# Optimization experiments

Hardware: AMD Instinct MI355X
Metric: run time of the kernel (lower is better)

## Reference

```python
import jax, jax.numpy as jnp
import numpy as np

N = 100000      # nodes
E = 400000      # edges (before self loops)
D_ATOM = 98
D_BOND = 13
EMB = 128
HEADS = 4
L = 4           # num_layer


def prelu(x, a):
    return jnp.where(x >= 0, x, a * x)


def setup_inputs() -> dict:
    key = jax.random.key(0)
    ks = jax.random.split(key, 12)
    s = 0.05
    inp = {
        "x": jax.random.normal(ks[0], (N, D_ATOM), dtype=jnp.float32),
        "edge_index": jax.random.randint(ks[1], (2, E), 0, N, dtype=jnp.int64),
        "edge_attr": jax.random.uniform(ks[2], (E, D_BOND), dtype=jnp.float32),
        # GNN-level params
        "x_emb_W": jax.random.normal(ks[3], (D_ATOM, EMB), dtype=jnp.float32) * s,
        "prelu_gnn": jnp.float32(0.25),
        # per-layer GATConv params, stacked on leading layer axis
        "wl_W": jax.random.normal(ks[4], (L, EMB, HEADS * EMB), dtype=jnp.float32) * s,
        "wl_b": jnp.zeros((L, HEADS * EMB), dtype=jnp.float32),
        "att": jax.random.normal(ks[5], (L, HEADS, 2 * EMB), dtype=jnp.float32) * s,
        "gat_bias": jnp.zeros((L, EMB), dtype=jnp.float32),
        "ee_W": jax.random.normal(ks[6], (L, D_BOND, HEADS * EMB), dtype=jnp.float32) * s,
        "ee_b": jnp.zeros((L, HEADS * EMB), dtype=jnp.float32),
        "prelu_gat": jnp.full((L,), 0.25, dtype=jnp.float32),
        # LayerNorm params per layer
        "ln_g": jnp.ones((L, EMB), dtype=jnp.float32),
        "ln_b": jnp.zeros((L, EMB), dtype=jnp.float32),
    }
    return inp


def reference(x, edge_index, edge_attr, x_emb_W, prelu_gnn, wl_W, wl_b, att,
              gat_bias, ee_W, ee_b, prelu_gat, ln_g, ln_b):
    # add self loops: (i, i) for every node; self-loop edge_attr = zeros
    loop = jnp.arange(N, dtype=edge_index.dtype)
    src = jnp.concatenate([edge_index[0], loop])  # [E+N] source (j)
    dst = jnp.concatenate([edge_index[1], loop])  # [E+N] target (i)
    ea = jnp.concatenate(
        [edge_attr, jnp.zeros((N, D_BOND), dtype=edge_attr.dtype)], axis=0)

    # input embedding + shared PReLU
    h = prelu(x @ x_emb_W, prelu_gnn)  # [N, EMB]

    for l in range(L):
        a = prelu_gat[l]
        ee = prelu(ea @ ee_W[l] + ee_b[l], a)       # [E+N, H*EMB]
        xw = prelu(h @ wl_W[l] + wl_b[l], a)        # [N, H*EMB]
        x_i = xw[dst].reshape(-1, HEADS, EMB)       # target feats
        x_j = (xw[src] + ee).reshape(-1, HEADS, EMB)  # source feats + edge emb
        # attention logits: cat([x_i,x_j]) . att
        alpha = (x_i * att[l, :, :EMB]).sum(-1) + (x_j * att[l, :, EMB:]).sum(-1)
        alpha = prelu(alpha, a)                     # [E+N, HEADS]
        # segment softmax grouped by src (edge_index[0]), as in the module
        m = jax.ops.segment_max(alpha, src, num_segments=N)
        alpha = jnp.exp(alpha - m[src])
        ssum = jax.ops.segment_sum(alpha, src, num_segments=N)
        alpha = alpha / (ssum[src] + 1e-16)
        # weighted messages, scatter-add to target nodes
        msg = (x_j * alpha[:, :, None]).reshape(-1, HEADS * EMB)
        aggr = jax.ops.segment_sum(msg, dst, num_segments=N)
        aggr = aggr.reshape(N, HEADS, EMB).mean(axis=1) + gat_bias[l]
        # LayerNorm
        mu = aggr.mean(-1, keepdims=True)
        var = ((aggr - mu) ** 2).mean(-1, keepdims=True)
        hn = (aggr - mu) / jnp.sqrt(var + 1e-5) * ln_g[l] + ln_b[l]
        # dropout is identity (drop_ratio=0); PReLU on all but last layer
        h = hn if l == L - 1 else prelu(hn, prelu_gnn)

    return h  # JK='last'
```

## Files before the change

kernel.cpp:

```cpp
#include <hip/hip_runtime.h>
#include <stdint.h>

#define NN 100000
#define NE 400000
#define NT 500000
#define DA 98
#define DB 13
#define EMB 128
#define HE 512
#define NWAVE 8192

typedef unsigned short ushort_t;
typedef __bf16 bf16x8 __attribute__((ext_vector_type(8)));
typedef float floatx4 __attribute__((ext_vector_type(4)));
typedef __fp16 fp16v2 __attribute__((ext_vector_type(2)));

__device__ __forceinline__ float prelu_f(float x, float a) { return x >= 0.f ? x : a * x; }

__device__ __forceinline__ ushort_t f2bf(float f) {
    unsigned u = __float_as_uint(f);
    unsigned r = (u + 0x7fffu + ((u >> 16) & 1u)) >> 16;
    return (ushort_t)r;
}
__device__ __forceinline__ float bflo(unsigned u) { return __uint_as_float(u << 16); }
__device__ __forceinline__ float bfhi(unsigned u) { return __uint_as_float(u & 0xffff0000u); }

__device__ __forceinline__ float dot2(unsigned a, unsigned b, float c) {
    return __builtin_amdgcn_fdot2(__builtin_bit_cast(fp16v2, a), __builtin_bit_cast(fp16v2, b), c, false);
}

__device__ __forceinline__ unsigned pk2(float lo, float hi) {
    fp16v2 p = __builtin_amdgcn_cvt_pkrtz(lo, hi);
    return __builtin_bit_cast(unsigned, p);
}

__global__ void k_count(const int* __restrict__ ei, int* __restrict__ sc, int* __restrict__ dc) {
    int e = blockIdx.x * 256 + threadIdx.x;
    if (e >= NT) return;
    int s, d;
    if (e < NE) { s = ei[e]; d = ei[NE + e]; } else { s = d = e - NE; }
    atomicAdd(sc + s, 1);
    atomicAdd(dc + d, 1);
}

__global__ void k_scan1(const int* __restrict__ cnt, int* __restrict__ part, int* __restrict__ bsum) {
    __shared__ int tmp[512];
    int t = threadIdx.x, i = blockIdx.x * 512 + t;
    int v = (i < NN) ? cnt[i] : 0;
    tmp[t] = v;
    __syncthreads();
    for (int off = 1; off < 512; off <<= 1) {
        int x = (t >= off) ? tmp[t - off] : 0;
        __syncthreads();
        tmp[t] += x;
        __syncthreads();
    }
    if (i < NN) part[i] = tmp[t] - v;
    if (t == 511) bsum[blockIdx.x] = tmp[t];
}

__global__ void k_scan2(int* __restrict__ bsum, int nb) {
    __shared__ int tmp[256];
    int t = threadIdx.x;
    int v = (t < nb) ? bsum[t] : 0;
    tmp[t] = v;
    __syncthreads();
    for (int off = 1; off < 256; off <<= 1) {
        int x = (t >= off) ? tmp[t - off] : 0;
        __syncthreads();
        tmp[t] += x;
        __syncthreads();
    }
    if (t < nb) bsum[t] = tmp[t] - v;
}

__global__ void k_scan3(const int* __restrict__ part, const int* __restrict__ bsum,
                        int* __restrict__ off, int* __restrict__ cur) {
    int i = blockIdx.x * 256 + threadIdx.x;
    if (i < NN) {
        int v = part[i] + bsum[i >> 9];
        off[i] = v;
        cur[i] = v;
    }
    if (i == 0) off[NN] = NT;
}

__global__ void k_fill(const int* __restrict__ ei, int* __restrict__ scur, int* __restrict__ dcur,
                       int* __restrict__ seid, int* __restrict__ deid) {
    int e = blockIdx.x * 256 + threadIdx.x;
    if (e >= NT) return;
    int s, d;
    if (e < NE) { s = ei[e]; d = ei[NE + e]; } else { s = d = e - NE; }
    seid[atomicAdd(scur + s, 1)] = e;
    deid[atomicAdd(dcur + d, 1)] = e;
}

__global__ void k_invperm(const int* __restrict__ seid, int* __restrict__ s2p) {
    int i = blockIdx.x * 256 + threadIdx.x;
    if (i < NT) s2p[seid[i]] = i;
}

__global__ void k_wrange(const int* __restrict__ doff, int* __restrict__ nstart) {
    int w = blockIdx.x * 256 + threadIdx.x;
    if (w > NWAVE) return;
    long long target = (long long)w * NT / NWAVE;
    int lo = 0, hi = NN;
    while (lo < hi) {
        int mid = (lo + hi) >> 1;
        if ((long long)doff[mid] < target) lo = mid + 1; else hi = mid;
    }
    nstart[w] = lo;
}

__global__ void k_dprep(const int* __restrict__ deid, const int* __restrict__ ei,
                        const float* __restrict__ ea, const int* __restrict__ s2p,
                        int* __restrict__ src_d, int* __restrict__ d2s,
                        unsigned* __restrict__ ea_d) {
    int i = blockIdx.x * 256 + threadIdx.x;
    if (i >= NT) return;
    int eid = deid[i];
    unsigned p[8] = {0, 0, 0, 0, 0, 0, 0, 0};
    int s;
    if (eid < NE) {
        s = ei[eid];
        float v[DB];
        #pragma unroll
        for (int k = 0; k < DB; ++k) v[k] = ea[(size_t)eid * DB + k];
        #pragma unroll
        for (int kp = 0; kp < 6; ++kp) p[kp] = pk2(v[2 * kp], v[2 * kp + 1]);
        p[6] = pk2(v[12], 0.f);
    } else {
        s = eid - NE;
    }
    uint4* o = (uint4*)&ea_d[(size_t)i * 8];
    o[0] = make_uint4(p[0], p[1], p[2], p[3]);
    o[1] = make_uint4(p[4], p[5], p[6], p[7]);
    src_d[i] = s;
    d2s[i] = s2p[eid];
}

__global__ __launch_bounds__(128) void k_embed(const float* __restrict__ x, const float* __restrict__ W,
                                               const float* __restrict__ pg, ushort_t* __restrict__ hb) {
    __shared__ float Ws[DA * EMB];
    __shared__ float xr[DA];
    int t = threadIdx.x;
    for (int i = t; i < DA * EMB; i += 128) Ws[i] = W[i];
    float p = pg[0];
    __syncthreads();
    for (int n = blockIdx.x; n < NN; n += gridDim.x) {
        if (t < DA) xr[t] = x[(size_t)n * DA + t];
        __syncthreads();
        float acc = 0.f;
        #pragma unroll
        for (int k = 0; k < DA; ++k) acc += xr[k] * Ws[k * EMB + t];
        hb[(size_t)n * EMB + t] = f2bf(prelu_f(acc, p));
        __syncthreads();
    }
}

__global__ void k_prep(const float* __restrict__ wlW, ushort_t* __restrict__ Wtg) {
    int idx = blockIdx.x * 256 + threadIdx.x;
    if (idx >= 4 * 512 * 128) return;
    int k = idx & 127;
    int n = (idx >> 7) & 511;
    int l = idx >> 16;
    Wtg[idx] = f2bf(wlW[(size_t)l * 65536 + k * 512 + n]);
}

__global__ void k_prep_eep(const float* __restrict__ eeW, unsigned* __restrict__ eeWp) {
    int idx = blockIdx.x * 256 + threadIdx.x;
    if (idx >= 4 * 7 * 512) return;
    int l = idx / 3584;
    int rem = idx - l * 3584;
    int kp = rem >> 9;
    int ch = rem & 511;
    float lo = eeW[((size_t)l * DB + 2 * kp) * HE + ch];
    float hi = (2 * kp + 1 < DB) ? eeW[((size_t)l * DB + 2 * kp + 1) * HE + ch] : 0.f;
    eeWp[idx] = pk2(lo, hi);
}

__global__ __launch_bounds__(256) void k_gemm(const ushort_t* __restrict__ hb, const ushort_t* __restrict__ Wtg,
                                              const float* __restrict__ bl, const float* __restrict__ pa,
                                              ushort_t* __restrict__ xw) {
    __shared__ ushort_t At[64 * 136];
    __shared__ ushort_t Bt[128 * 136];
    int t = threadIdx.x;
    int m0 = blockIdx.x * 64;
    int n0 = blockIdx.y * 128;
    for (int idx = t; idx < 64 * 16; idx += 256) {
        int r = idx >> 4, co = (idx & 15) * 8;
        int gr = m0 + r; if (gr >= NN) gr = 0;
        *(uint4*)&At[r * 136 + co] = *(const uint4*)&hb[(size_t)gr * EMB + co];
    }
    for (int idx = t; idx < 128 * 16; idx += 256) {
        int n = idx >> 4, ko = (idx & 15) * 8;
        *(uint4*)&Bt[n * 136 + ko] = *(const uint4*)&Wtg[(size_t)(n0 + n) * 128 + ko];
    }
    float a = pa[0];
    __syncthreads();

    int wv = t >> 6, lane = t & 63;
    int ml = lane & 15, kq = lane >> 4;
    int n0w = wv * 32;
    floatx4 acc[4][2];
    #pragma unroll
    for (int mt = 0; mt < 4; ++mt)
        #pragma unroll
        for (int nt = 0; nt < 2; ++nt)
            acc[mt][nt] = (floatx4){0.f, 0.f, 0.f, 0.f};

    #pragma unroll
    for (int k0 = 0; k0 < 128; k0 += 32) {
        bf16x8 af[4], bfv[2];
        #pragma unroll
        for (int mt = 0; mt < 4; ++mt) {
            uint4 u = *(const uint4*)&At[(mt * 16 + ml) * 136 + k0 + kq * 8];
            af[mt] = __builtin_bit_cast(bf16x8, u);
        }
        #pragma unroll
        for (int nt = 0; nt < 2; ++nt) {
            uint4 u = *(const uint4*)&Bt[(n0w + nt * 16 + ml) * 136 + k0 + kq * 8];
            bfv[nt] = __builtin_bit_cast(bf16x8, u);
        }
        #pragma unroll
        for (int mt = 0; mt < 4; ++mt)
            #pragma unroll
            for (int nt = 0; nt < 2; ++nt)
                acc[mt][nt] = __builtin_amdgcn_mfma_f32_16x16x32_bf16(af[mt], bfv[nt], acc[mt][nt], 0, 0, 0);
    }
    #pragma unroll
    for (int nt = 0; nt < 2; ++nt) {
        int col = n0 + n0w + nt * 16 + ml;
        float bv = bl[col];
        #pragma unroll
        for (int mt = 0; mt < 4; ++mt) {
            int row = m0 + mt * 16 + kq * 4;
            #pragma unroll
            for (int q = 0; q < 4; ++q) {
                int r = row + q;
                if (r < NN) xw[(size_t)r * HE + col] = f2bf(prelu_f(acc[mt][nt][q] + bv, a));
            }
        }
    }
}

__global__ __launch_bounds__(256) void k_dots(const ushort_t* __restrict__ xw,
                                              const float* __restrict__ attl,
                                              float* __restrict__ ddst, float* __restrict__ dsrc) {
    int t = threadIdx.x;
    int lane = t & 63;
    int wid = blockIdx.x * 4 + (t >> 6);
    int nw = gridDim.x * 4;
    int hd = lane >> 4;
    int cm = (lane & 15) * 8;
    float a1[8], a2[8];
    #pragma unroll
    for (int q = 0; q < 8; ++q) {
        a1[q] = attl[hd * 256 + cm + q];
        a2[q] = attl[hd * 256 + 128 + cm + q];
    }
    for (int n = wid; n < NN; n += nw) {
        uint4 u = *(const uint4*)&xw[(size_t)n * HE + lane * 8];
        float v[8] = {bflo(u.x), bfhi(u.x), bflo(u.y), bfhi(u.y),
                      bflo(u.z), bfhi(u.z), bflo(u.w), bfhi(u.w)};
        float p1 = 0.f, p2 = 0.f;
        #pragma unroll
        for (int q = 0; q < 8; ++q) { p1 += v[q] * a1[q]; p2 += v[q] * a2[q]; }
        #pragma unroll
        for (int m = 1; m < 16; m <<= 1) {
            p1 += __shfl_xor(p1, m, 64);
            p2 += __shfl_xor(p2, m, 64);
        }
        if ((lane & 15) == 0) {
            ddst[n * 4 + hd] = p1;
            dsrc[n * 4 + hd] = p2;
        }
    }
}

__global__ __launch_bounds__(256) void k_edge(const int* __restrict__ ei, const float* __restrict__ ea,
                                              const unsigned* __restrict__ eeWp, const float* __restrict__ ebl,
                                              const float* __restrict__ attl, const float* __restrict__ pa,
                                              const float* __restrict__ ddst, const float* __restrict__ dsrc,
                                              const int* __restrict__ s2p,
                                              float* __restrict__ alpha_s) {
    int t = threadIdx.x;
    float a = pa[0];
    int lane = t & 63;
    int wid = blockIdx.x * 4 + (t >> 6);
    int nw = gridDim.x * 4;
    int hd = lane >> 4;
    int cm = (lane & 15) * 8;
    int c0 = lane * 8;
    uint4 wpa[7], wpb[7];
    #pragma unroll
    for (int kp = 0; kp < 7; ++kp) {
        wpa[kp] = *(const uint4*)&eeWp[kp * HE + c0];
        wpb[kp] = *(const uint4*)&eeWp[kp * HE + c0 + 4];
    }
    float a2[8], eb[8];
    #pragma unroll
    for (int q = 0; q < 8; ++q) {
        a2[q] = attl[hd * 256 + 128 + cm + q];
        eb[q] = ebl[c0 + q];
    }
    float pself = 0.f;
    #pragma unroll
    for (int q = 0; q < 8; ++q) pself += prelu_f(eb[q], a) * a2[q];
    for (int e = wid; e < NT; e += nw) {
        int s, d;
        float p;
        if (e < NE) {
            s = ei[e]; d = ei[NE + e];
            float eav[DB];
            #pragma unroll
            for (int k = 0; k < DB; ++k) eav[k] = ea[(size_t)e * DB + k];
            unsigned ep[7];
            #pragma unroll
            for (int kp = 0; kp < 6; ++kp) ep[kp] = pk2(eav[2 * kp], eav[2 * kp + 1]);
            ep[6] = pk2(eav[12], 0.f);
            float v[8];
            #pragma unroll
            for (int q = 0; q < 8; ++q) v[q] = eb[q];
            #pragma unroll
            for (int kp = 0; kp < 7; ++kp) {
                v[0] = dot2(ep[kp], wpa[kp].x, v[0]);
                v[1] = dot2(ep[kp], wpa[kp].y, v[1]);
                v[2] = dot2(ep[kp], wpa[kp].z, v[2]);
                v[3] = dot2(ep[kp], wpa[kp].w, v[3]);
                v[4] = dot2(ep[kp], wpb[kp].x, v[4]);
                v[5] = dot2(ep[kp], wpb[kp].y, v[5]);
                v[6] = dot2(ep[kp], wpb[kp].z, v[6]);
                v[7] = dot2(ep[kp], wpb[kp].w, v[7]);
            }
            p = 0.f;
            #pragma unroll
            for (int q = 0; q < 8; ++q) p += prelu_f(v[q], a) * a2[q];
        } else {
            s = d = e - NE;
            p = pself;
        }
        #pragma unroll
        for (int m = 1; m < 16; m <<= 1) p += __shfl_xor(p, m, 64);
        if ((lane & 15) == 0) {
            int sp = s2p[e];
            float di = ddst[d * 4 + hd];
            float sj = dsrc[s * 4 + hd];
            alpha_s[(size_t)sp * 4 + hd] = prelu_f(di + sj + p, a);
        }
    }
}

__global__ void k_softmax(const int* __restrict__ soff, float4* __restrict__ alpha_s) {
    int n = blockIdx.x * 256 + threadIdx.x;
    if (n >= NN) return;
    int b = soff[n], e = soff[n + 1];
    float mx = -1e30f, my = -1e30f, mz = -1e30f, mw = -1e30f;
    for (int i = b; i < e; ++i) {
        float4 v = alpha_s[i];
        mx = fmaxf(mx, v.x); my = fmaxf(my, v.y);
        mz = fmaxf(mz, v.z); mw = fmaxf(mw, v.w);
    }
    float sx = 0.f, sy = 0.f, sz = 0.f, sw = 0.f;
    for (int i = b; i < e; ++i) {
        float4 v = alpha_s[i];
        v.x = __expf(v.x - mx); v.y = __expf(v.y - my);
        v.z = __expf(v.z - mz); v.w = __expf(v.w - mw);
        sx += v.x; sy += v.y; sz += v.z; sw += v.w;
        alpha_s[i] = v;
    }
    sx = 1.f / (sx + 1e-16f); sy = 1.f / (sy + 1e-16f);
    sz = 1.f / (sz + 1e-16f); sw = 1.f / (sw + 1e-16f);
    for (int i = b; i < e; ++i) {
        float4 v = alpha_s[i];
        v.x *= sx; v.y *= sy; v.z *= sz; v.w *= sw;
        alpha_s[i] = v;
    }
}

__global__ __launch_bounds__(256) void k_aggr(const int* __restrict__ nstart,
                                              const int* __restrict__ doff,
                                              const int* __restrict__ src_d, const int* __restrict__ d2s,
                                              const unsigned* __restrict__ ea_d,
                                              const unsigned* __restrict__ eeWp, const float* __restrict__ ebl,
                                              const float* __restrict__ pa, const ushort_t* __restrict__ xw,
                                              const float* __restrict__ alpha_s,
                                              const float* __restrict__ gbias, const float* __restrict__ lng,
                                              const float* __restrict__ lnb, const float* __restrict__ pgnn,
                                              int last, ushort_t* __restrict__ hb_out, float* __restrict__ fout) {
    int t = threadIdx.x;
    float a = pa[0], pg = pgnn[0];
    int lane = t & 63;
    int w = blockIdx.x * 4 + (t >> 6);
    int hd = lane >> 4;
    int cm = (lane & 15) * 8;
    int c0 = lane * 8;
    uint4 wpa[7], wpb[7];
    #pragma unroll
    for (int kp = 0; kp < 7; ++kp) {
        wpa[kp] = *(const uint4*)&eeWp[kp * HE + c0];
        wpb[kp] = *(const uint4*)&eeWp[kp * HE + c0 + 4];
    }
    float eb[8];
    #pragma unroll
    for (int q = 0; q < 8; ++q) eb[q] = ebl[c0 + q];

    int n0 = nstart[w], n1 = nstart[w + 1];
    if (n0 >= n1) return;
    int e0 = doff[n0];
    int e1 = doff[n1];
    int li = e1 - 1;

    int i1 = (e0 + 1 <= li) ? e0 + 1 : li;
    int i2 = (e0 + 2 <= li) ? e0 + 2 : li;
    int sA = src_d[e0], pA = d2s[e0];
    int sB = src_d[i1], pB = d2s[i1];
    uint4 xwA = *(const uint4*)&xw[(size_t)sA * HE + c0];
    float alA = alpha_s[(size_t)pA * 4 + hd];
    uint4 xwB = *(const uint4*)&xw[(size_t)sB * HE + c0];
    float alB = alpha_s[(size_t)pB * 4 + hd];
    int sN = src_d[i2], pN = d2s[i2];
    uint4 eaCa = *(const uint4*)&ea_d[(size_t)e0 * 8];
    uint4 eaCb = *(const uint4*)&ea_d[(size_t)e0 * 8 + 4];

    int n = n0;
    int b1 = doff[n0 + 1];
    int nn2 = (n0 + 2 <= NN) ? n0 + 2 : NN;
    int b2 = doff[nn2];
    float acc[8] = {0.f, 0.f, 0.f, 0.f, 0.f, 0.f, 0.f, 0.f};

    for (int i = e0; i < e1; ++i) {
        int ip = (i + 1 <= li) ? i + 1 : li;
        uint4 eaNa = *(const uint4*)&ea_d[(size_t)ip * 8];
        uint4 eaNb = *(const uint4*)&ea_d[(size_t)ip * 8 + 4];
        uint4 xwC = *(const uint4*)&xw[(size_t)sN * HE + c0];
        float alC = alpha_s[(size_t)pN * 4 + hd];
        int i3 = (i + 3 <= li) ? i + 3 : li;
        int sN2 = src_d[i3], pN2 = d2s[i3];
        unsigned ec[7] = {eaCa.x, eaCa.y, eaCa.z, eaCa.w, eaCb.x, eaCb.y, eaCb.z};
        float wv[8];
        #pragma unroll
        for (int q = 0; q < 8; ++q) wv[q] = eb[q];
        #pragma unroll
        for (int kp = 0; kp < 7; ++kp) {
            wv[0] = dot2(ec[kp], wpa[kp].x, wv[0]);
            wv[1] = dot2(ec[kp], wpa[kp].y, wv[1]);
            wv[2] = dot2(ec[kp], wpa[kp].z, wv[2]);
            wv[3] = dot2(ec[kp], wpa[kp].w, wv[3]);
            wv[4] = dot2(ec[kp], wpb[kp].x, wv[4]);
            wv[5] = dot2(ec[kp], wpb[kp].y, wv[5]);
            wv[6] = dot2(ec[kp], wpb[kp].z, wv[6]);
            wv[7] = dot2(ec[kp], wpb[kp].w, wv[7]);
        }
        float xv[8] = {bflo(xwA.x), bfhi(xwA.x), bflo(xwA.y), bfhi(xwA.y),
                       bflo(xwA.z), bfhi(xwA.z), bflo(xwA.w), bfhi(xwA.w)};
        #pragma unroll
        for (int q = 0; q < 8; ++q) acc[q] += (xv[q] + prelu_f(wv[q], a)) * alA;
        if (i + 1 == b1) {
            float gbv[8], gv[8], bbv[8];
            *(float4*)&gbv[0] = *(const float4*)&gbias[cm];
            *(float4*)&gbv[4] = *(const float4*)&gbias[cm + 4];
            *(float4*)&gv[0]  = *(const float4*)&lng[cm];
            *(float4*)&gv[4]  = *(const float4*)&lng[cm + 4];
            *(float4*)&bbv[0] = *(const float4*)&lnb[cm];
            *(float4*)&bbv[4] = *(const float4*)&lnb[cm + 4];
            float hm[8];
            #pragma unroll
            for (int q = 0; q < 8; ++q) {
                float v = acc[q];
                v += __shfl_xor(v, 16, 64);
                v += __shfl_xor(v, 32, 64);
                hm[q] = 0.25f * v + gbv[q];
            }
            float s8 = 0.f, q8 = 0.f;
            #pragma unroll
            for (int q = 0; q < 8; ++q) { s8 += hm[q]; q8 += hm[q] * hm[q]; }
            #pragma unroll
            for (int m = 1; m < 16; m <<= 1) {
                s8 += __shfl_xor(s8, m, 64);
                q8 += __shfl_xor(q8, m, 64);
            }
            float mu = s8 * (1.f / 128.f);
            float var = q8 * (1.f / 128.f) - mu * mu;
            float rstd = rsqrtf(var + 1e-5f);
            if (lane < 16) {
                float o[8];
                #pragma unroll
                for (int q = 0; q < 8; ++q) {
                    float v = (hm[q] - mu) * rstd * gv[q] + bbv[q];
                    o[q] = last ? v : prelu_f(v, pg);
                }
                if (last) {
                    float4* op = (float4*)&fout[(size_t)n * EMB + lane * 8];
                    op[0] = make_float4(o[0], o[1], o[2], o[3]);
                    op[1] = make_float4(o[4], o[5], o[6], o[7]);
                } else {
                    uint4 ob;
                    ob.x = (unsigned)f2bf(o[0]) | ((unsigned)f2bf(o[1]) << 16);
                    ob.y = (unsigned)f2bf(o[2]) | ((unsigned)f2bf(o[3]) << 16);
                    ob.z = (unsigned)f2bf(o[4]) | ((unsigned)f2bf(o[5]) << 16);
                    ob.w = (unsigned)f2bf(o[6]) | ((unsigned)f2bf(o[7]) << 16);
                    *(uint4*)&hb_out[(size_t)n * EMB + lane * 8] = ob;
                }
            }
            #pragma unroll
            for (int q = 0; q < 8; ++q) acc[q] = 0.f;
            ++n;
            b1 = b2;
            int nx = (n + 2 <= NN) ? n + 2 : NN;
            b2 = doff[nx];
        }
        xwA = xwB; alA = alB;
        xwB = xwC; alB = alC;
        sN = sN2; pN = pN2;
        eaCa = eaNa; eaCb = eaNb;
    }
}

extern "C" void kernel_launch(void* const* d_in, const int* in_sizes, int n_in,
                              void* d_out, int out_size, void* d_ws, size_t ws_size,
                              hipStream_t stream) {
    const float* x     = (const float*)d_in[0];
    const int*   ei    = (const int*)d_in[1];
    const float* ea    = (const float*)d_in[2];
    const float* xembW = (const float*)d_in[3];
    const float* pgnn  = (const float*)d_in[4];
    const float* wlW   = (const float*)d_in[5];
    const float* wlb   = (const float*)d_in[6];
    const float* att   = (const float*)d_in[7];
    const float* gbias = (const float*)d_in[8];
    const float* eeW   = (const float*)d_in[9];
    const float* eeb   = (const float*)d_in[10];
    const float* pgat  = (const float*)d_in[11];
    const float* lng   = (const float*)d_in[12];
    const float* lnb   = (const float*)d_in[13];

    char* w = (char*)d_ws;
    size_t off = 0;
    auto alloc = [&](size_t nbytes) -> char* {
        char* p = w + off;
        off += (nbytes + 255) & ~(size_t)255;
        return p;
    };
    ushort_t* hb    = (ushort_t*)alloc((size_t)NN * EMB * 2);
    ushort_t* xw    = (ushort_t*)alloc((size_t)NN * HE * 2);
    ushort_t* Wtg   = (ushort_t*)alloc((size_t)4 * 512 * 128 * 2);
    unsigned* eeWp  = (unsigned*)alloc((size_t)4 * 7 * 512 * 4);
    float*    ddst  = (float*)alloc((size_t)NN * 4 * 4);
    float*    dsrc  = (float*)alloc((size_t)NN * 4 * 4);
    float*    alpha = (float*)alloc((size_t)NT * 4 * 4);
    unsigned* ea_d  = (unsigned*)alloc((size_t)NT * 8 * 4);
    int* scnt   = (int*)alloc((size_t)NN * 4);
    int* dcnt   = (int*)alloc((size_t)NN * 4);
    int* soff   = (int*)alloc((size_t)(NN + 1) * 4);
    int* doff   = (int*)alloc((size_t)(NN + 1) * 4);
    int* scur   = (int*)alloc((size_t)NN * 4);
    int* dcur   = (int*)alloc((size_t)NN * 4);
    int* seid   = (int*)alloc((size_t)NT * 4);
    int* deid   = (int*)alloc((size_t)NT * 4);
    int* s2p    = (int*)alloc((size_t)NT * 4);
    int* src_d  = (int*)alloc((size_t)NT * 4);
    int* d2s    = (int*)alloc((size_t)NT * 4);
    int* nstart = (int*)alloc((size_t)(NWAVE + 1) * 4);
    int* part   = (int*)alloc((size_t)NN * 4);
    int* bsum   = (int*)alloc(256 * 4);

    hipMemsetAsync(scnt, 0, (size_t)NN * 4, stream);
    hipMemsetAsync(dcnt, 0, (size_t)NN * 4, stream);
    k_count<<<(NT + 255) / 256, 256, 0, stream>>>(ei, scnt, dcnt);
    k_scan1<<<196, 512, 0, stream>>>(scnt, part, bsum);
    k_scan2<<<1, 256, 0, stream>>>(bsum, 196);
    k_scan3<<<391, 256, 0, stream>>>(part, bsum, soff, scur);
    k_scan1<<<196, 512, 0, stream>>>(dcnt, part, bsum);
    k_scan2<<<1, 256, 0, stream>>>(bsum, 196);
    k_scan3<<<391, 256, 0, stream>>>(part, bsum, doff, dcur);
    k_fill<<<(NT + 255) / 256, 256, 0, stream>>>(ei, scur, dcur, seid, deid);
    k_invperm<<<(NT + 255) / 256, 256, 0, stream>>>(seid, s2p);
    k_wrange<<<(NWAVE + 1 + 255) / 256, 256, 0, stream>>>(doff, nstart);
    k_dprep<<<(NT + 255) / 256, 256, 0, stream>>>(deid, ei, ea, s2p, src_d, d2s, ea_d);
    k_embed<<<2048, 128, 0, stream>>>(x, xembW, pgnn, hb);
    k_prep<<<(4 * 512 * 128 + 255) / 256, 256, 0, stream>>>(wlW, Wtg);
    k_prep_eep<<<(4 * 7 * 512 + 255) / 256, 256, 0, stream>>>(eeW, eeWp);

    for (int l = 0; l < 4; ++l) {
        const float* bl  = wlb + (size_t)l * HE;
        const float* al  = att + (size_t)l * 1024;
        const unsigned* eWl = eeWp + (size_t)l * 7 * HE;
        const float* ebl = eeb + (size_t)l * HE;
        const float* pa  = pgat + l;
        const ushort_t* Wt = Wtg + (size_t)l * 512 * 128;
        k_gemm<<<dim3((NN + 63) / 64, 4), 256, 0, stream>>>(hb, Wt, bl, pa, xw);
        k_dots<<<2048, 256, 0, stream>>>(xw, al, ddst, dsrc);
        k_edge<<<2048, 256, 0, stream>>>(ei, ea, eWl, ebl, al, pa, ddst, dsrc, s2p, alpha);
        k_softmax<<<391, 256, 0, stream>>>(soff, (float4*)alpha);
        k_aggr<<<2048, 256, 0, stream>>>(nstart, doff, src_d, d2s, ea_d, eWl, ebl, pa, xw, alpha,
                                         gbias + (size_t)l * EMB, lng + (size_t)l * EMB,
                                         lnb + (size_t)l * EMB, pgnn, (l == 3) ? 1 : 0,
                                         hb, (float*)d_out);
    }
}
```

Baseline: 2.112 ms.

## Use MFMA for input embedding and fuse attention dot products into GEMM epilogue

Replaces the scalar fp32 embedding kernel with a bf16 MFMA GEMM, adding prep kernels that zero-pad x and the embedding weight to K=128. It also removes the separate k_dots kernel by computing the per-head attention dot products in the k_gemm epilogue, using shuffles plus a shared-memory reduction across waves. This avoids re-reading xw each layer and cuts one launch per layer. In exchange the embedding input is now rounded to bf16, and the dots use unrounded fp32 values rather than the stored bf16 ones.

```diff
diff --git a/kernel.cpp b/kernel.cpp
--- a/kernel.cpp
+++ b/kernel.cpp
@@ -139,22 +139,81 @@
     d2s[i] = s2p[eid];
 }
 
-__global__ __launch_bounds__(128) void k_embed(const float* __restrict__ x, const float* __restrict__ W,
-                                               const float* __restrict__ pg, ushort_t* __restrict__ hb) {
-    __shared__ float Ws[DA * EMB];
-    __shared__ float xr[DA];
+__global__ void k_prep_x(const float* __restrict__ x, ushort_t* __restrict__ xb) {
+    int idx = blockIdx.x * 256 + threadIdx.x;
+    if (idx >= NN * 128) return;
+    int col = idx & 127, n = idx >> 7;
+    float v = (col < DA) ? x[(size_t)n * DA + col] : 0.f;
+    xb[idx] = f2bf(v);
+}
+
+__global__ void k_prep_wx(const float* __restrict__ W, ushort_t* __restrict__ Wxt) {
+    int idx = blockIdx.x * 256 + threadIdx.x;
+    if (idx >= 128 * 128) return;
+    int k = idx & 127, n = idx >> 7;
+    float v = (k < DA) ? W[(size_t)k * EMB + n] : 0.f;
+    Wxt[idx] = f2bf(v);
+}
+
+__global__ __launch_bounds__(256) void k_embed_m(const ushort_t* __restrict__ xb, const ushort_t* __restrict__ Wxt,
+                                                 const float* __restrict__ pg, ushort_t* __restrict__ hb) {
+    __shared__ ushort_t At[64 * 136];
+    __shared__ ushort_t Bt[128 * 136];
     int t = threadIdx.x;
-    for (int i = t; i < DA * EMB; i += 128) Ws[i] = W[i];
+    int m0 = blockIdx.x * 64;
+    for (int idx = t; idx < 64 * 16; idx += 256) {
+        int r = idx >> 4, co = (idx & 15) * 8;
+        int gr = m0 + r; if (gr >= NN) gr = 0;
+        *(uint4*)&At[r * 136 + co] = *(const uint4*)&xb[(size_t)gr * 128 + co];
+    }
+    for (int idx = t; idx < 128 * 16; idx += 256) {
+        int n = idx >> 4, ko = (idx & 15) * 8;
+        *(uint4*)&Bt[n * 136 + ko] = *(const uint4*)&Wxt[n * 128 + ko];
+    }
     float p = pg[0];
     __syncthreads();
-    for (int n = blockIdx.x; n < NN; n += gridDim.x) {
-        if (t < DA) xr[t] = x[(size_t)n * DA + t];
-        __syncthreads();
-        float acc = 0.f;
-        #pragma unroll
-        for (int k = 0; k < DA; ++k) acc += xr[k] * Ws[k * EMB + t];
-        hb[(size_t)n * EMB + t] = f2bf(prelu_f(acc, p));
-        __syncthreads();
+
+    int wv = t >> 6, lane = t & 63;
+    int ml = lane & 15, kq = lane >> 4;
+    int n0w = wv * 32;
+    floatx4 acc[4][2];
+    #pragma unroll
+    for (int mt = 0; mt < 4; ++mt)
+        #pragma unroll
+        for (int nt = 0; nt < 2; ++nt)
+            acc[mt][nt] = (floatx4){0.f, 0.f, 0.f, 0.f};
+
+    #pragma unroll
+    for (int k0 = 0; k0 < 128; k0 += 32) {
+        bf16x8 af[4], bfv[2];
+        #pragma unroll
+        for (int mt = 0; mt < 4; ++mt) {
+            uint4 u = *(const uint4*)&At[(mt * 16 + ml) * 136 + k0 + kq * 8];
+            af[mt] = __builtin_bit_cast(bf16x8, u);
+        }
+        #pragma unroll
+        for (int nt = 0; nt < 2; ++nt) {
+            uint4 u = *(const uint4*)&Bt[(n0w + nt * 16 + ml) * 136 + k0 + kq * 8];
+            bfv[nt] = __builtin_bit_cast(bf16x8, u);
+        }
+        #pragma unroll
+        for (int mt = 0; mt < 4; ++mt)
+            #pragma unroll
+            for (int nt = 0; nt < 2; ++nt)
+                acc[mt][nt] = __builtin_amdgcn_mfma_f32_16x16x32_bf16(af[mt], bfv[nt], acc[mt][nt], 0, 0, 0);
+    }
+    #pragma unroll
+    for (int nt = 0; nt < 2; ++nt) {
+        int col = n0w + nt * 16 + ml;
+        #pragma unroll
+        for (int mt = 0; mt < 4; ++mt) {
+            int row = m0 + mt * 16 + kq * 4;
+            #pragma unroll
+            for (int q = 0; q < 4; ++q) {
+                int r = row + q;
+                if (r < NN) hb[(size_t)r * EMB + col] = f2bf(prelu_f(acc[mt][nt][q], p));
+            }
+        }
     }
 }
 
@@ -181,12 +240,15 @@
 
 __global__ __launch_bounds__(256) void k_gemm(const ushort_t* __restrict__ hb, const ushort_t* __restrict__ Wtg,
                                               const float* __restrict__ bl, const float* __restrict__ pa,
-                                              ushort_t* __restrict__ xw) {
+                                              const float* __restrict__ attl,
+                                              ushort_t* __restrict__ xw,
+                                              float* __restrict__ ddst, float* __restrict__ dsrc) {
     __shared__ ushort_t At[64 * 136];
     __shared__ ushort_t Bt[128 * 136];
     int t = threadIdx.x;
     int m0 = blockIdx.x * 64;
-    int n0 = blockIdx.y * 128;
+    int h = blockIdx.y;
+    int n0 = h * 128;
     for (int idx = t; idx < 64 * 16; idx += 256) {
         int r = idx >> 4, co = (idx & 15) * 8;
         int gr = m0 + r; if (gr >= NN) gr = 0;
@@ -228,52 +290,60 @@
             for (int nt = 0; nt < 2; ++nt)
                 acc[mt][nt] = __builtin_amdgcn_mfma_f32_16x16x32_bf16(af[mt], bfv[nt], acc[mt][nt], 0, 0, 0);
     }
+    __syncthreads();
+    float* sdd = (float*)At;
+    float* sds = (float*)At + 256;
+
+    float pd[4][4], ps[4][4];
+    #pragma unroll
+    for (int mt = 0; mt < 4; ++mt)
+        #pragma unroll
+        for (int q = 0; q < 4; ++q) { pd[mt][q] = 0.f; ps[mt][q] = 0.f; }
+
     #pragma unroll
     for (int nt = 0; nt < 2; ++nt) {
-        int col = n0 + n0w + nt * 16 + ml;
+        int ch = n0w + nt * 16 + ml;
+        int col = n0 + ch;
         float bv = bl[col];
+        float a1v = attl[h * 256 + ch];
+        float a2v = attl[h * 256 + 128 + ch];
         #pragma unroll
         for (int mt = 0; mt < 4; ++mt) {
             int row = m0 + mt * 16 + kq * 4;
             #pragma unroll
             for (int q = 0; q < 4; ++q) {
                 int r = row + q;
-                if (r < NN) xw[(size_t)r * HE + col] = f2bf(prelu_f(acc[mt][nt][q] + bv, a));
-            }
-        }
-    }
-}
-
-__global__ __launch_bounds__(256) void k_dots(const ushort_t* __restrict__ xw,
-                                              const float* __restrict__ attl,
-                                              float* __restrict__ ddst, float* __restrict__ dsrc) {
-    int t = threadIdx.x;
-    int lane = t & 63;
-    int wid = blockIdx.x * 4 + (t >> 6);
-    int nw = gridDim.x * 4;
-    int hd = lane >> 4;
-    int cm = (lane & 15) * 8;
-    float a1[8], a2[8];
-    #pragma unroll
-    for (int q = 0; q < 8; ++q) {
-        a1[q] = attl[hd * 256 + cm + q];
-        a2[q] = attl[hd * 256 + 128 + cm + q];
-    }
-    for (int n = wid; n < NN; n += nw) {
-        uint4 u = *(const uint4*)&xw[(size_t)n * HE + lane * 8];
-        float v[8] = {bflo(u.x), bfhi(u.x), bflo(u.y), bfhi(u.y),
-                      bflo(u.z), bfhi(u.z), bflo(u.w), bfhi(u.w)};
-        float p1 = 0.f, p2 = 0.f;
-        #pragma unroll
-        for (int q = 0; q < 8; ++q) { p1 += v[q] * a1[q]; p2 += v[q] * a2[q]; }
-        #pragma unroll
-        for (int m = 1; m < 16; m <<= 1) {
-            p1 += __shfl_xor(p1, m, 64);
-            p2 += __shfl_xor(p2, m, 64);
-        }
-        if ((lane & 15) == 0) {
-            ddst[n * 4 + hd] = p1;
-            dsrc[n * 4 + hd] = p2;
+                float v = prelu_f(acc[mt][nt][q] + bv, a);
+                if (r < NN) xw[(size_t)r * HE + col] = f2bf(v);
+                pd[mt][q] += v * a1v;
+                ps[mt][q] += v * a2v;
+            }
+        }
+    }
+    #pragma unroll
+    for (int mt = 0; mt < 4; ++mt)
+        #pragma unroll
+        for (int q = 0; q < 4; ++q) {
+            float d = pd[mt][q], s = ps[mt][q];
+            #pragma unroll
+            for (int m = 1; m < 16; m <<= 1) {
+                d += __shfl_xor(d, m, 64);
+                s += __shfl_xor(s, m, 64);
+            }
+            if (ml == 0) {
+                int lr = mt * 16 + kq * 4 + q;
+                sdd[wv * 64 + lr] = d;
+                sds[wv * 64 + lr] = s;
+            }
+        }
+    __syncthreads();
+    if (t < 64) {
+        int r = m0 + t;
+        if (r < NN) {
+            float d = sdd[t] + sdd[64 + t] + sdd[128 + t] + sdd[192 + t];
+            float s = sds[t] + sds[64 + t] + sds[128 + t] + sds[192 + t];
+            ddst[r * 4 + h] = d;
+            dsrc[r * 4 + h] = s;
         }
     }
 }
@@ -545,6 +615,7 @@
     ushort_t* hb    = (ushort_t*)alloc((size_t)NN * EMB * 2);
     ushort_t* xw    = (ushort_t*)alloc((size_t)NN * HE * 2);
     ushort_t* Wtg   = (ushort_t*)alloc((size_t)4 * 512 * 128 * 2);
+    ushort_t* Wxt   = (ushort_t*)alloc((size_t)128 * 128 * 2);
     unsigned* eeWp  = (unsigned*)alloc((size_t)4 * 7 * 512 * 4);
     float*    ddst  = (float*)alloc((size_t)NN * 4 * 4);
     float*    dsrc  = (float*)alloc((size_t)NN * 4 * 4);
@@ -565,6 +636,8 @@
     int* part   = (int*)alloc((size_t)NN * 4);
     int* bsum   = (int*)alloc(256 * 4);
 
+    ushort_t* xb = xw;
+
     hipMemsetAsync(scnt, 0, (size_t)NN * 4, stream);
     hipMemsetAsync(dcnt, 0, (size_t)NN * 4, stream);
     k_count<<<(NT + 255) / 256, 256, 0, stream>>>(ei, scnt, dcnt);
@@ -578,7 +651,9 @@
     k_invperm<<<(NT + 255) / 256, 256, 0, stream>>>(seid, s2p);
     k_wrange<<<(NWAVE + 1 + 255) / 256, 256, 0, stream>>>(doff, nstart);
     k_dprep<<<(NT + 255) / 256, 256, 0, stream>>>(deid, ei, ea, s2p, src_d, d2s, ea_d);
-    k_embed<<<2048, 128, 0, stream>>>(x, xembW, pgnn, hb);
+    k_prep_x<<<(NN * 128 + 255) / 256, 256, 0, stream>>>(x, xb);
+    k_prep_wx<<<(128 * 128 + 255) / 256, 256, 0, stream>>>(xembW, Wxt);
+    k_embed_m<<<(NN + 63) / 64, 256, 0, stream>>>(xb, Wxt, pgnn, hb);
     k_prep<<<(4 * 512 * 128 + 255) / 256, 256, 0, stream>>>(wlW, Wtg);
     k_prep_eep<<<(4 * 7 * 512 + 255) / 256, 256, 0, stream>>>(eeW, eeWp);
 
@@ -589,8 +664,7 @@
         const float* ebl = eeb + (size_t)l * HE;
         const float* pa  = pgat + l;
         const ushort_t* Wt = Wtg + (size_t)l * 512 * 128;
-        k_gemm<<<dim3((NN + 63) / 64, 4), 256, 0, stream>>>(hb, Wt, bl, pa, xw);
-        k_dots<<<2048, 256, 0, stream>>>(xw, al, ddst, dsrc);
+        k_gemm<<<dim3((NN + 63) / 64, 4), 256, 0, stream>>>(hb, Wt, bl, pa, al, xw, ddst, dsrc);
         k_edge<<<2048, 256, 0, stream>>>(ei, ea, eWl, ebl, al, pa, ddst, dsrc, s2p, alpha);
         k_softmax<<<391, 256, 0, stream>>>(soff, (float4*)alpha);
         k_aggr<<<2048, 256, 0, stream>>>(nstart, doff, src_d, d2s, ea_d, eWl, ebl, pa, xw, alpha,
```

Measured after the change: 1.921 ms. 1.1x faster.
